# Kernel tuning notes

Measured on AMD Instinct MI355X. Metric: run time of the kernel, lower is better.

The kernel has to match this reference:

```python
import jax, jax.numpy as jnp
import numpy as np

BUCKET_SIZE = 64  # must divide seq_len


def setup_inputs() -> dict:
    key = jax.random.key(0)
    k1, k2, k3, k4 = jax.random.split(key, 4)
    B, S, D = 4, 4096, 1024
    query = jax.random.normal(k1, (B, S, D), dtype=jnp.float32)
    key_t = jax.random.normal(k2, (B, S, D), dtype=jnp.float32)
    value = jax.random.normal(k3, (B, S, D), dtype=jnp.float32)
    # random hashing hyperplanes: [B, D, bucket_size // 2]
    R = jax.random.normal(k4, (B, D, BUCKET_SIZE // 2), dtype=jnp.float32)
    return {"query": query, "key": key_t, "value": value, "R": R}


def reference(query, key, value, R):
    B, S, D = query.shape
    # random projection: [B, S, bucket_size // 2]
    xR = jnp.einsum("bsd,bdr->bsr", query, R)
    # mirror trick -> [B, S, bucket_size]
    concat_xR = jnp.concatenate([xR, -xR], axis=-1)
    buckets = jnp.argmax(concat_xR, axis=-1)          # [B, S] int
    sticker = jnp.argsort(buckets, axis=-1)            # token permutation into buckets
    undo_sort = jnp.argsort(sticker, axis=-1)          # computed in original (unused)
    # batched gather (tf.gather batch_dims=1, axis=1)
    sorted_query = jnp.take_along_axis(query, sticker[..., None], axis=1)
    sorted_value = jnp.take_along_axis(value, sticker[..., None], axis=1)
    # tf.split(x, bucket_size, 1) then stack(axis=1) == reshape to chunks
    chunked_query = sorted_query.reshape(B, BUCKET_SIZE, S // BUCKET_SIZE, D)
    chunked_value = sorted_value.reshape(B, BUCKET_SIZE, S // BUCKET_SIZE, D)
    del undo_sort, chunked_query, chunked_value  # dead code in original; module returns sticker
    return sticker
```

## Files before the change

### kernel.cpp

```cpp
#include <hip/hip_runtime.h>


#define B_DIM 4
#define S_LEN 4096
#define D_DIM 1024
#define NRR 32
#define NBK 64
#define TMK 16
#define NCH (S_LEN / TMK)
#define NT 8

typedef const __attribute__((address_space(1))) void* gas_t;
typedef __attribute__((address_space(3))) void* las_t;

__global__ void __launch_bounds__(256) __attribute__((amdgpu_waves_per_eu(4, 4)))
k1_buckets(const float* __restrict__ Q, const float* __restrict__ R,
           int* __restrict__ buckets, int* __restrict__ hist)
{
    __shared__ float4 smem4[3072];
    __shared__ float xs[TMK * 33];
    __shared__ int cnt[NBK];

    const int t = threadIdx.x;
    const int b = blockIdx.x >> 8;
    const int ch = blockIdx.x & 255;

    const int w = t >> 6;
    const int lane = t & 63;
    const int tok_t = lane >> 5;
    const int r_t = (lane >> 3) & 3;
    const int kl = lane & 7;
    const int kq = w * 8 + kl;
    const int dwb = t & ~63;
    const int rsw0 = (r_t * 2 + 0) ^ kl;
    const int rsw1 = (r_t * 2 + 1) ^ kl;
    const int qoff = tok_t * 256 + kq;
    const int roff = kq * 32;

    const float4* Qg4 = (const float4*)(Q + ((size_t)b * S_LEN + ch * TMK) * D_DIM);
    const float4* Rg4 = (const float4*)(R + (size_t)b * D_DIM * NRR);

#define ISSUE(TILE, D)                                                        \
    {                                                                         \
        _Pragma("unroll")                                                     \
        for (int i = 0; i < 2; ++i) {                                         \
            const int f = t + 256 * i;                                        \
            __builtin_amdgcn_global_load_lds(                                 \
                (gas_t)(Qg4 + (size_t)(f >> 5) * 256 + (TILE) * 32 + (f & 31)),\
                (las_t)&smem4[(D) * 512 + (i << 8) + dwb], 16, 0, 0);         \
        }                                                                     \
        _Pragma("unroll")                                                     \
        for (int i = 0; i < 4; ++i) {                                         \
            const int f = t + 256 * i;                                        \
            __builtin_amdgcn_global_load_lds(                                 \
                (gas_t)(Rg4 + ((size_t)(TILE) * 128 + (f >> 3)) * 8           \
                        + ((f & 7) ^ ((f >> 5) & 7))),                        \
                (las_t)&smem4[1024 + (D) * 1024 + (i << 8) + dwb], 16, 0, 0); \
        }                                                                     \
    }

#define COMPUTE(D)                                                            \
    {                                                                         \
        const float4* qb = smem4 + (D) * 512;                                 \
        const float4* rb = smem4 + 1024 + (D) * 1024;                         \
        float4 rv[4][2];                                                      \
        _Pragma("unroll")                                                     \
        for (int kk = 0; kk < 4; ++kk) {                                      \
            rv[kk][0] = rb[roff + kk * 8 + rsw0];                             \
            rv[kk][1] = rb[roff + kk * 8 + rsw1];                             \
        }                                                                     \
        _Pragma("unroll")                                                     \
        for (int j = 0; j < 8; ++j) {                                         \
            const float4 qv = qb[qoff + j * 32];                              \
            _Pragma("unroll")                                                 \
            for (int kk = 0; kk < 4; ++kk) {                                  \
                const float s = kk == 0 ? qv.x : kk == 1 ? qv.y               \
                              : kk == 2 ? qv.z : qv.w;                        \
                _Pragma("unroll")                                             \
                for (int p = 0; p < 2; ++p) {                                 \
                    acc[j][p].x = fmaf(s, rv[kk][p].x, acc[j][p].x);          \
                    acc[j][p].y = fmaf(s, rv[kk][p].y, acc[j][p].y);          \
                    acc[j][p].z = fmaf(s, rv[kk][p].z, acc[j][p].z);          \
                    acc[j][p].w = fmaf(s, rv[kk][p].w, acc[j][p].w);          \
                }                                                             \
            }                                                                 \
        }                                                                     \
    }

    float4 acc[8][2];
#pragma unroll
    for (int j = 0; j < 8; ++j) {
        acc[j][0] = make_float4(0.f, 0.f, 0.f, 0.f);
        acc[j][1] = make_float4(0.f, 0.f, 0.f, 0.f);
    }

    ISSUE(0, 0)
    for (int tau = 0; tau < NT; ++tau) {
        if (tau + 1 < NT) {
            ISSUE(tau + 1, (tau + 1) & 1)
            asm volatile("s_waitcnt vmcnt(6)\n\ts_barrier" ::: "memory");
        } else {
            asm volatile("s_waitcnt vmcnt(0)\n\ts_barrier" ::: "memory");
        }
        COMPUTE(tau & 1)
        if (tau + 1 < NT) {
            asm volatile("s_waitcnt lgkmcnt(0)\n\ts_barrier" ::: "memory");
        } else {
            __syncthreads();
        }
    }
#undef ISSUE
#undef COMPUTE

#pragma unroll
    for (int j = 0; j < 8; ++j)
#pragma unroll
        for (int p = 0; p < 2; ++p) {
#pragma unroll
            for (int off = 1; off < 8; off <<= 1) {
                acc[j][p].x += __shfl_xor(acc[j][p].x, off, 64);
                acc[j][p].y += __shfl_xor(acc[j][p].y, off, 64);
                acc[j][p].z += __shfl_xor(acc[j][p].z, off, 64);
                acc[j][p].w += __shfl_xor(acc[j][p].w, off, 64);
            }
        }

    if (t < NBK) cnt[t] = 0;
    if (kl == 0) {
#pragma unroll
        for (int j = 0; j < 8; ++j) {
            const int tok = tok_t * 8 + j;
            smem4[w * 128 + tok * 8 + r_t * 2 + 0] = acc[j][0];
            smem4[w * 128 + tok * 8 + r_t * 2 + 1] = acc[j][1];
        }
    }
    __syncthreads();

    if (t < 128) {
        float4 s = smem4[t];
#pragma unroll
        for (int ww = 1; ww < 4; ++ww) {
            const float4 v = smem4[ww * 128 + t];
            s.x += v.x; s.y += v.y; s.z += v.z; s.w += v.w;
        }
        const int tok = t >> 3, rq = t & 7;
        xs[tok * 33 + rq * 4 + 0] = s.x;
        xs[tok * 33 + rq * 4 + 1] = s.y;
        xs[tok * 33 + rq * 4 + 2] = s.z;
        xs[tok * 33 + rq * 4 + 3] = s.w;
    }
    __syncthreads();

    if (t < TMK) {
        float m1 = xs[t * 33 + 0]; int i1 = 0;
        float m2 = m1;             int i2 = 0;
#pragma unroll
        for (int r = 1; r < NRR; ++r) {
            const float v = xs[t * 33 + r];
            if (v > m1) { m1 = v; i1 = r; }
            if (v < m2) { m2 = v; i2 = r; }
        }
        const int bk = (m1 >= -m2) ? i1 : (NRR + i2);
        buckets[(size_t)b * S_LEN + ch * TMK + t] = bk;
        atomicAdd(&cnt[bk], 1);
    }
    __syncthreads();
    if (t < NBK) hist[((size_t)b * NCH + ch) * NBK + t] = cnt[t];
}

__global__ __launch_bounds__(256) void k2_scan(
    const int* __restrict__ hist, int* __restrict__ chunkOffset)
{
    const int t = threadIdx.x;
    const int b = t >> 6;
    const int bk = t & 63;
    const int lane = t & 63;

    int total = 0;
    for (int c = 0; c < NCH; ++c)
        total += hist[((size_t)b * NCH + c) * NBK + bk];

    int incl = total;
#pragma unroll
    for (int off = 1; off < 64; off <<= 1) {
        int n = __shfl_up(incl, off, 64);
        if (lane >= off) incl += n;
    }
    int run = incl - total;

    for (int c = 0; c < NCH; ++c) {
        int h = hist[((size_t)b * NCH + c) * NBK + bk];
        chunkOffset[((size_t)b * NCH + c) * NBK + bk] = run;
        run += h;
    }
}

__global__ __launch_bounds__(256) void k3_scatter(
    const int* __restrict__ buckets, const int* __restrict__ chunkOffset,
    int* __restrict__ out)
{
    const int gid = blockIdx.x * 256 + threadIdx.x;
    const int b = gid >> 12;
    const int s = gid & (S_LEN - 1);
    const int chunk = s >> 4;
    const int lane = threadIdx.x & 63;

    const int bk = buckets[gid];

    unsigned long long m = ~0ull;
#pragma unroll
    for (int i = 0; i < 6; ++i) {
        unsigned long long bi = __ballot((bk >> i) & 1);
        m &= ((bk >> i) & 1) ? bi : ~bi;
    }
    const unsigned int m16 = (unsigned int)((m >> (lane & 48)) & 0xFFFFull);
    const int rank = __popc(m16 & ((1u << (lane & 15)) - 1u));

    const int pos = chunkOffset[((size_t)b * NCH + chunk) * NBK + bk] + rank;
    out[(size_t)b * S_LEN + pos] = s;
}

extern "C" void kernel_launch(void* const* d_in, const int* in_sizes, int n_in,
                              void* d_out, int out_size, void* d_ws, size_t ws_size,
                              hipStream_t stream) {
    const float* Q = (const float*)d_in[0];
    const float* R = (const float*)d_in[3];

    int* buckets     = (int*)d_ws;
    int* hist        = buckets + B_DIM * S_LEN;
    int* chunkOffset = hist + B_DIM * NCH * NBK;

    k1_buckets<<<B_DIM * NCH, 256, 0, stream>>>(Q, R, buckets, hist);
    k2_scan   <<<1,           256, 0, stream>>>(hist, chunkOffset);
    k3_scatter<<<(B_DIM * S_LEN) / 256, 256, 0, stream>>>(buckets, chunkOffset, (int*)d_out);
}
```

Baseline: 48.91 us.

## Double token tile per block to 32 with 512-thread blocks sharing R tiles

The bucket-projection kernel now handles 32 tokens per block with 512 threads, two token groups by four k-slices, so each staged R tile in LDS serves twice as many query rows. The block count halves and per-block LDS grows. The histogram chunk becomes 32 tokens, which halves the serial loop length in the single-block scan kernel. The scatter ranks tokens within 32-lane half-wave masks. The cost is fewer, larger blocks, which may reduce occupancy and latency hiding.

```diff
diff --git a/kernel.cpp b/kernel.cpp
--- a/kernel.cpp
+++ b/kernel.cpp
@@ -6,63 +6,65 @@
 #define D_DIM 1024
 #define NRR 32
 #define NBK 64
-#define TMK 16
-#define NCH (S_LEN / TMK)
+#define TMK 32
+#define NC32 (S_LEN / TMK)
 #define NT 8
 
 typedef const __attribute__((address_space(1))) void* gas_t;
 typedef __attribute__((address_space(3))) void* las_t;
 
-__global__ void __launch_bounds__(256) __attribute__((amdgpu_waves_per_eu(4, 4)))
+__global__ void __launch_bounds__(512) __attribute__((amdgpu_waves_per_eu(4, 4)))
 k1_buckets(const float* __restrict__ Q, const float* __restrict__ R,
            int* __restrict__ buckets, int* __restrict__ hist)
 {
-    __shared__ float4 smem4[3072];
+    __shared__ float4 smem4[4096];
     __shared__ float xs[TMK * 33];
     __shared__ int cnt[NBK];
 
     const int t = threadIdx.x;
-    const int b = blockIdx.x >> 8;
-    const int ch = blockIdx.x & 255;
+    const int b = blockIdx.x >> 7;
+    const int c32 = blockIdx.x & 127;
 
     const int w = t >> 6;
     const int lane = t & 63;
+    const int wt = w >> 2;
+    const int wk = w & 3;
     const int tok_t = lane >> 5;
     const int r_t = (lane >> 3) & 3;
     const int kl = lane & 7;
-    const int kq = w * 8 + kl;
+    const int kq = wk * 8 + kl;
     const int dwb = t & ~63;
     const int rsw0 = (r_t * 2 + 0) ^ kl;
     const int rsw1 = (r_t * 2 + 1) ^ kl;
-    const int qoff = tok_t * 256 + kq;
+    const int qoff = (wt * 16 + tok_t * 8) * 32 + kq;
     const int roff = kq * 32;
 
-    const float4* Qg4 = (const float4*)(Q + ((size_t)b * S_LEN + ch * TMK) * D_DIM);
+    const float4* Qg4 = (const float4*)(Q + ((size_t)b * S_LEN + c32 * TMK) * D_DIM);
     const float4* Rg4 = (const float4*)(R + (size_t)b * D_DIM * NRR);
 
 #define ISSUE(TILE, D)                                                        \
     {                                                                         \
         _Pragma("unroll")                                                     \
         for (int i = 0; i < 2; ++i) {                                         \
-            const int f = t + 256 * i;                                        \
+            const int f = t + 512 * i;                    \
             __builtin_amdgcn_global_load_lds(                                 \
                 (gas_t)(Qg4 + (size_t)(f >> 5) * 256 + (TILE) * 32 + (f & 31)),\
-                (las_t)&smem4[(D) * 512 + (i << 8) + dwb], 16, 0, 0);         \
-        }                                                                     \
-        _Pragma("unroll")                                                     \
-        for (int i = 0; i < 4; ++i) {                                         \
-            const int f = t + 256 * i;                                        \
+                (las_t)&smem4[(D) * 1024 + (i * 512) + dwb], 16, 0, 0);       \
+        }                                                                     \
+        _Pragma("unroll")                                                     \
+        for (int i = 0; i < 2; ++i) {                                         \
+            const int f = t + 512 * i;                    \
             __builtin_amdgcn_global_load_lds(                                 \
                 (gas_t)(Rg4 + ((size_t)(TILE) * 128 + (f >> 3)) * 8           \
                         + ((f & 7) ^ ((f >> 5) & 7))),                        \
-                (las_t)&smem4[1024 + (D) * 1024 + (i << 8) + dwb], 16, 0, 0); \
+                (las_t)&smem4[2048 + (D) * 1024 + (i * 512) + dwb], 16, 0, 0);\
         }                                                                     \
     }
 
 #define COMPUTE(D)                                                            \
     {                                                                         \
-        const float4* qb = smem4 + (D) * 512;                                 \
-        const float4* rb = smem4 + 1024 + (D) * 1024;                         \
+        const float4* qb = smem4 + (D) * 1024;                                \
+        const float4* rb = smem4 + 2048 + (D) * 1024;                         \
         float4 rv[4][2];                                                      \
         _Pragma("unroll")                                                     \
         for (int kk = 0; kk < 4; ++kk) {                                      \
@@ -93,21 +95,18 @@
         acc[j][0] = make_float4(0.f, 0.f, 0.f, 0.f);
         acc[j][1] = make_float4(0.f, 0.f, 0.f, 0.f);
     }
+    if (t < NBK) cnt[t] = 0;
 
     ISSUE(0, 0)
     for (int tau = 0; tau < NT; ++tau) {
         if (tau + 1 < NT) {
             ISSUE(tau + 1, (tau + 1) & 1)
-            asm volatile("s_waitcnt vmcnt(6)\n\ts_barrier" ::: "memory");
+            asm volatile("s_waitcnt vmcnt(4)\n\ts_barrier" ::: "memory");
         } else {
             asm volatile("s_waitcnt vmcnt(0)\n\ts_barrier" ::: "memory");
         }
         COMPUTE(tau & 1)
-        if (tau + 1 < NT) {
-            asm volatile("s_waitcnt lgkmcnt(0)\n\ts_barrier" ::: "memory");
-        } else {
-            __syncthreads();
-        }
+        asm volatile("s_waitcnt lgkmcnt(0)\n\ts_barrier" ::: "memory");
     }
 #undef ISSUE
 #undef COMPUTE
@@ -124,23 +123,23 @@
                 acc[j][p].w += __shfl_xor(acc[j][p].w, off, 64);
             }
         }
-
-    if (t < NBK) cnt[t] = 0;
+    __syncthreads();
+
     if (kl == 0) {
 #pragma unroll
         for (int j = 0; j < 8; ++j) {
-            const int tok = tok_t * 8 + j;
-            smem4[w * 128 + tok * 8 + r_t * 2 + 0] = acc[j][0];
-            smem4[w * 128 + tok * 8 + r_t * 2 + 1] = acc[j][1];
-        }
-    }
-    __syncthreads();
-
-    if (t < 128) {
+            const int tok = wt * 16 + tok_t * 8 + j;
+            smem4[wk * 256 + tok * 8 + r_t * 2 + 0] = acc[j][0];
+            smem4[wk * 256 + tok * 8 + r_t * 2 + 1] = acc[j][1];
+        }
+    }
+    __syncthreads();
+
+    if (t < 256) {
         float4 s = smem4[t];
 #pragma unroll
         for (int ww = 1; ww < 4; ++ww) {
-            const float4 v = smem4[ww * 128 + t];
+            const float4 v = smem4[ww * 256 + t];
             s.x += v.x; s.y += v.y; s.z += v.z; s.w += v.w;
         }
         const int tok = t >> 3, rq = t & 7;
@@ -161,11 +160,11 @@
             if (v < m2) { m2 = v; i2 = r; }
         }
         const int bk = (m1 >= -m2) ? i1 : (NRR + i2);
-        buckets[(size_t)b * S_LEN + ch * TMK + t] = bk;
+        buckets[(size_t)b * S_LEN + c32 * TMK + t] = bk;
         atomicAdd(&cnt[bk], 1);
     }
     __syncthreads();
-    if (t < NBK) hist[((size_t)b * NCH + ch) * NBK + t] = cnt[t];
+    if (t < NBK) hist[((size_t)b * NC32 + c32) * NBK + t] = cnt[t];
 }
 
 __global__ __launch_bounds__(256) void k2_scan(
@@ -177,8 +176,8 @@
     const int lane = t & 63;
 
     int total = 0;
-    for (int c = 0; c < NCH; ++c)
-        total += hist[((size_t)b * NCH + c) * NBK + bk];
+    for (int c = 0; c < NC32; ++c)
+        total += hist[((size_t)b * NC32 + c) * NBK + bk];
 
     int incl = total;
 #pragma unroll
@@ -188,9 +187,9 @@
     }
     int run = incl - total;
 
-    for (int c = 0; c < NCH; ++c) {
-        int h = hist[((size_t)b * NCH + c) * NBK + bk];
-        chunkOffset[((size_t)b * NCH + c) * NBK + bk] = run;
+    for (int c = 0; c < NC32; ++c) {
+        int h = hist[((size_t)b * NC32 + c) * NBK + bk];
+        chunkOffset[((size_t)b * NC32 + c) * NBK + bk] = run;
         run += h;
     }
 }
@@ -202,7 +201,7 @@
     const int gid = blockIdx.x * 256 + threadIdx.x;
     const int b = gid >> 12;
     const int s = gid & (S_LEN - 1);
-    const int chunk = s >> 4;
+    const int chunk = s >> 5;
     const int lane = threadIdx.x & 63;
 
     const int bk = buckets[gid];
@@ -213,10 +212,10 @@
         unsigned long long bi = __ballot((bk >> i) & 1);
         m &= ((bk >> i) & 1) ? bi : ~bi;
     }
-    const unsigned int m16 = (unsigned int)((m >> (lane & 48)) & 0xFFFFull);
-    const int rank = __popc(m16 & ((1u << (lane & 15)) - 1u));
-
-    const int pos = chunkOffset[((size_t)b * NCH + chunk) * NBK + bk] + rank;
+    const unsigned int m32 = (unsigned int)(m >> (lane & 32));
+    const int rank = __popc(m32 & ((1u << (lane & 31)) - 1u));
+
+    const int pos = chunkOffset[((size_t)b * NC32 + chunk) * NBK + bk] + rank;
     out[(size_t)b * S_LEN + pos] = s;
 }
 
@@ -228,9 +227,9 @@
 
     int* buckets     = (int*)d_ws;
     int* hist        = buckets + B_DIM * S_LEN;
-    int* chunkOffset = hist + B_DIM * NCH * NBK;
-
-    k1_buckets<<<B_DIM * NCH, 256, 0, stream>>>(Q, R, buckets, hist);
-    k2_scan   <<<1,           256, 0, stream>>>(hist, chunkOffset);
+    int* chunkOffset = hist + B_DIM * NC32 * NBK;
+
+    k1_buckets<<<B_DIM * NC32, 512, 0, stream>>>(Q, R, buckets, hist);
+    k2_scan   <<<1,            256, 0, stream>>>(hist, chunkOffset);
     k3_scatter<<<(B_DIM * S_LEN) / 256, 256, 0, stream>>>(buckets, chunkOffset, (int*)d_out);
 }
```

Result: faster. 46.83 us (-4.3%).

## Load Q tiles directly into registers, stage only R through LDS

Applied to the files above, without the earlier changes.

Q fragments are now read from global memory straight into registers each tile instead of being staged through LDS with async global_load_lds, so only the R hyperplanes stay double-buffered in shared memory. This shrinks the LDS footprint and removes the LDS round-trip for Q, and the waves_per_eu hint is relaxed to allow 2-4 waves. In exchange, every tile now waits for both the Q register loads and the next R prefetch (vmcnt(0)) before its barrier, so Q loads overlap less with compute. The histogram counter initialization moves earlier in the kernel.

```diff
diff --git a/kernel.cpp b/kernel.cpp
--- a/kernel.cpp
+++ b/kernel.cpp
@@ -13,11 +13,11 @@
 typedef const __attribute__((address_space(1))) void* gas_t;
 typedef __attribute__((address_space(3))) void* las_t;
 
-__global__ void __launch_bounds__(256) __attribute__((amdgpu_waves_per_eu(4, 4)))
+__global__ void __launch_bounds__(256) __attribute__((amdgpu_waves_per_eu(2, 4)))
 k1_buckets(const float* __restrict__ Q, const float* __restrict__ R,
            int* __restrict__ buckets, int* __restrict__ hist)
 {
-    __shared__ float4 smem4[3072];
+    __shared__ float4 smem4[2048];
     __shared__ float xs[TMK * 33];
     __shared__ int cnt[NBK];
 
@@ -34,56 +34,20 @@
     const int dwb = t & ~63;
     const int rsw0 = (r_t * 2 + 0) ^ kl;
     const int rsw1 = (r_t * 2 + 1) ^ kl;
-    const int qoff = tok_t * 256 + kq;
     const int roff = kq * 32;
 
     const float4* Qg4 = (const float4*)(Q + ((size_t)b * S_LEN + ch * TMK) * D_DIM);
     const float4* Rg4 = (const float4*)(R + (size_t)b * D_DIM * NRR);
 
-#define ISSUE(TILE, D)                                                        \
+#define ISSUE_R(TILE, D)                                                      \
     {                                                                         \
-        _Pragma("unroll")                                                     \
-        for (int i = 0; i < 2; ++i) {                                         \
-            const int f = t + 256 * i;                                        \
-            __builtin_amdgcn_global_load_lds(                                 \
-                (gas_t)(Qg4 + (size_t)(f >> 5) * 256 + (TILE) * 32 + (f & 31)),\
-                (las_t)&smem4[(D) * 512 + (i << 8) + dwb], 16, 0, 0);         \
-        }                                                                     \
         _Pragma("unroll")                                                     \
         for (int i = 0; i < 4; ++i) {                                         \
             const int f = t + 256 * i;                                        \
             __builtin_amdgcn_global_load_lds(                                 \
                 (gas_t)(Rg4 + ((size_t)(TILE) * 128 + (f >> 3)) * 8           \
                         + ((f & 7) ^ ((f >> 5) & 7))),                        \
-                (las_t)&smem4[1024 + (D) * 1024 + (i << 8) + dwb], 16, 0, 0); \
-        }                                                                     \
-    }
-
-#define COMPUTE(D)                                                            \
-    {                                                                         \
-        const float4* qb = smem4 + (D) * 512;                                 \
-        const float4* rb = smem4 + 1024 + (D) * 1024;                         \
-        float4 rv[4][2];                                                      \
-        _Pragma("unroll")                                                     \
-        for (int kk = 0; kk < 4; ++kk) {                                      \
-            rv[kk][0] = rb[roff + kk * 8 + rsw0];                             \
-            rv[kk][1] = rb[roff + kk * 8 + rsw1];                             \
-        }                                                                     \
-        _Pragma("unroll")                                                     \
-        for (int j = 0; j < 8; ++j) {                                         \
-            const float4 qv = qb[qoff + j * 32];                              \
-            _Pragma("unroll")                                                 \
-            for (int kk = 0; kk < 4; ++kk) {                                  \
-                const float s = kk == 0 ? qv.x : kk == 1 ? qv.y               \
-                              : kk == 2 ? qv.z : qv.w;                        \
-                _Pragma("unroll")                                             \
-                for (int p = 0; p < 2; ++p) {                                 \
-                    acc[j][p].x = fmaf(s, rv[kk][p].x, acc[j][p].x);          \
-                    acc[j][p].y = fmaf(s, rv[kk][p].y, acc[j][p].y);          \
-                    acc[j][p].z = fmaf(s, rv[kk][p].z, acc[j][p].z);          \
-                    acc[j][p].w = fmaf(s, rv[kk][p].w, acc[j][p].w);          \
-                }                                                             \
-            }                                                                 \
+                (las_t)&smem4[(D) * 1024 + (i << 8) + dwb], 16, 0, 0);        \
         }                                                                     \
     }
 
@@ -93,24 +57,46 @@
         acc[j][0] = make_float4(0.f, 0.f, 0.f, 0.f);
         acc[j][1] = make_float4(0.f, 0.f, 0.f, 0.f);
     }
-
-    ISSUE(0, 0)
+    if (t < NBK) cnt[t] = 0;
+
+    ISSUE_R(0, 0)
+    asm volatile("s_waitcnt vmcnt(0)\n\ts_barrier" ::: "memory");
+
     for (int tau = 0; tau < NT; ++tau) {
-        if (tau + 1 < NT) {
-            ISSUE(tau + 1, (tau + 1) & 1)
-            asm volatile("s_waitcnt vmcnt(6)\n\ts_barrier" ::: "memory");
-        } else {
-            asm volatile("s_waitcnt vmcnt(0)\n\ts_barrier" ::: "memory");
-        }
-        COMPUTE(tau & 1)
-        if (tau + 1 < NT) {
-            asm volatile("s_waitcnt lgkmcnt(0)\n\ts_barrier" ::: "memory");
-        } else {
-            __syncthreads();
-        }
-    }
-#undef ISSUE
-#undef COMPUTE
+        float4 qv[8];
+#pragma unroll
+        for (int j = 0; j < 8; ++j)
+            qv[j] = Qg4[(size_t)(tok_t * 8 + j) * 256 + tau * 32 + kq];
+
+        if (tau + 1 < NT) ISSUE_R(tau + 1, (tau + 1) & 1)
+
+        {
+            const float4* rb = smem4 + (tau & 1) * 1024;
+            float4 rv[4][2];
+#pragma unroll
+            for (int kk = 0; kk < 4; ++kk) {
+                rv[kk][0] = rb[roff + kk * 8 + rsw0];
+                rv[kk][1] = rb[roff + kk * 8 + rsw1];
+            }
+#pragma unroll
+            for (int j = 0; j < 8; ++j) {
+#pragma unroll
+                for (int kk = 0; kk < 4; ++kk) {
+                    const float s = kk == 0 ? qv[j].x : kk == 1 ? qv[j].y
+                                  : kk == 2 ? qv[j].z : qv[j].w;
+#pragma unroll
+                    for (int p = 0; p < 2; ++p) {
+                        acc[j][p].x = fmaf(s, rv[kk][p].x, acc[j][p].x);
+                        acc[j][p].y = fmaf(s, rv[kk][p].y, acc[j][p].y);
+                        acc[j][p].z = fmaf(s, rv[kk][p].z, acc[j][p].z);
+                        acc[j][p].w = fmaf(s, rv[kk][p].w, acc[j][p].w);
+                    }
+                }
+            }
+        }
+        asm volatile("s_waitcnt vmcnt(0) lgkmcnt(0)\n\ts_barrier" ::: "memory");
+    }
+#undef ISSUE_R
 
 #pragma unroll
     for (int j = 0; j < 8; ++j)
@@ -125,7 +111,6 @@
             }
         }
 
-    if (t < NBK) cnt[t] = 0;
     if (kl == 0) {
 #pragma unroll
         for (int j = 0; j < 8; ++j) {
```

New measurement: 49.45 us. Within noise of the previous version (+1.1%).
